# Kernel tuning notes

Measured on AMD Instinct MI355X. Metric: run time of the kernel, lower is better.

## Reference

```python
import jax, jax.numpy as jnp
import numpy as np

NX, NY, NZ = 128, 128, 8
N_VOX = NX * NY * NZ
V, C, HF, WF = 6, 64, 116, 200
PAD_H, PAD_W = 928.0, 1600.0  # img_pad_shape (input image after padding)
IMG_H, IMG_W = 928.0, 1600.0  # img_shape used for the valid-flag bounds check


def _make_proj_mats():
    # Structured lidar2img matrices: pinhole intrinsics + 6 yaw-distributed cameras.
    K = np.array([[500.0, 0, 400, 0], [0, 500.0, 232, 0], [0, 0, 1, 0], [0, 0, 0, 1]], dtype=np.float64)
    A = np.array([[0.0, -1, 0], [0, 0, -1], [1, 0, 0]], dtype=np.float64)  # lidar(x fwd,y left,z up)->cam(z fwd)
    mats = []
    for j in range(V):
        yaw = 2.0 * np.pi * j / V
        c, s = np.cos(yaw), np.sin(yaw)
        Rz = np.array([[c, s, 0], [-s, c, 0], [0, 0, 1]])
        T = np.eye(4)
        T[:3, :3] = A @ Rz
        T[:3, 3] = np.array([0.0, -1.0, 0.0])
        mats.append(K @ T)
    return jnp.asarray(np.stack(mats), dtype=jnp.float32)


def setup_inputs() -> dict:
    key = jax.random.key(0)
    k1, k2 = jax.random.split(key)
    x_fov = jax.random.normal(k1, (1, V, C, HF, WF), dtype=jnp.float32)
    lo = jnp.array([-50.0, -50.0, -5.0], jnp.float32)
    span = jnp.array([100.0, 100.0, 8.0], jnp.float32)
    points = jax.random.uniform(k2, (N_VOX, 3), dtype=jnp.float32) * span + lo
    proj_mats = _make_proj_mats()
    return {"x_fov": x_fov, "points": points, "proj_mats": proj_mats}


def _bilinear_sample(feat, px, py):
    # feat [C,HF,WF]; px/py [N] in feature-map pixel coords.
    # Matches F.grid_sample(mode='bilinear', padding_mode='zeros', align_corners=False).
    x0 = jnp.floor(px)
    y0 = jnp.floor(py)
    wx1 = px - x0
    wy1 = py - y0

    def gather(xi, yi, w):
        inb = (xi >= 0) & (xi < WF) & (yi >= 0) & (yi < HF)
        xc = jnp.clip(xi, 0, WF - 1).astype(jnp.int32)
        yc = jnp.clip(yi, 0, HF - 1).astype(jnp.int32)
        return feat[:, yc, xc] * (w * inb)[None, :]  # [C,N]

    return (gather(x0, y0, (1 - wx1) * (1 - wy1))
            + gather(x0 + 1, y0, wx1 * (1 - wy1))
            + gather(x0, y0 + 1, (1 - wx1) * wy1)
            + gather(x0 + 1, y0 + 1, wx1 * wy1))


def _forward(x_fov, points, proj_mats):
    n = points.shape[0]
    # points_cam2img: homogeneous projection, perspective divide
    pts_h = jnp.concatenate([points, jnp.ones((n, 1), points.dtype)], axis=-1)  # [N,4]
    cam = jnp.einsum('vij,nj->vni', proj_mats, pts_h)  # [V,N,4]
    depth = cam[..., 2]
    d_safe = jnp.where(jnp.abs(depth) > 1e-6, depth, 1e-6)
    u = cam[..., 0] / d_safe  # image-plane x in input-image pixels (scale=1, crop=0, no flip)
    v = cam[..., 1] / d_safe
    # valid_flag: in front of camera and inside img_shape
    valid = (depth > 0) & (u > 0) & (u < IMG_W) & (v > 0) & (v < IMG_H)  # [V,N]
    # normalize by img_pad_shape then map to feature-map pixels (align_corners=False)
    px = u / PAD_W * WF - 0.5
    py = v / PAD_H * HF - 0.5
    feats = jax.vmap(_bilinear_sample)(x_fov[0], px, py)  # [V,C,N]
    feats = feats * valid[:, None, :].astype(feats.dtype)
    vol = feats.sum(0)  # [C,N] masked sum over views
    cnt = valid.sum(0).astype(feats.dtype)  # [N]
    vol = jnp.where(cnt > 0, vol, 0.0) / jnp.clip(cnt, 0.001)[None, :]
    # reshape(n_voxels[::-1] + [-1]).permute(3,2,1,0) -> [C,NX,NY,NZ]
    out = jnp.transpose(vol.reshape(C, NZ, NY, NX), (0, 3, 2, 1))
    return out[None]  # [1,C,NX,NY,NZ]


def reference(x_fov, points, proj_mats):
    return _forward(x_fov, points, proj_mats)
```

## Files before the change

### kernel.cpp

```cpp
#include <hip/hip_runtime.h>
#include <hip/hip_bf16.h>
#include <hip/hip_fp16.h>

#define NXv 128
#define NYv 128
#define NZv 8
#define NVOX (NXv * NYv * NZv)
#define NV 6
#define NC 64
#define HFv 116
#define WFv 200
#define PLANE (HFv * WFv)

#define FT_BYTES ((size_t)NV * PLANE * NC * 2)

typedef float v2f __attribute__((ext_vector_type(2)));

__device__ inline unsigned int f2bf(float f) {
  unsigned int x = __float_as_uint(f);
  unsigned int r = x + 0x7fffu + ((x >> 16) & 1u);
  return (r >> 16) & 0xffffu;
}
__device__ inline float bf_lo(unsigned int q) { return __uint_as_float(q << 16); }
__device__ inline float bf_hi(unsigned int q) { return __uint_as_float(q & 0xffff0000u); }
__device__ inline v2f bfpair(unsigned int u) {
  v2f r;
  r.x = __uint_as_float(u << 16);
  r.y = __uint_as_float(u & 0xffff0000u);
  return r;
}

__device__ inline unsigned short f2h_bits(float f) {
  __half h = __float2half(f);
  return *reinterpret_cast<unsigned short*>(&h);
}
__device__ inline float h_bits2f(unsigned short u) {
  __half_raw r; r.x = u;
  __half h = *reinterpret_cast<__half*>(&r);
  return __half2float(h);
}

__global__ __launch_bounds__(256) void transpose_feat_bf16(
    const float* __restrict__ in, unsigned int* __restrict__ out32) {
  __shared__ float tile[64][65];
  const int v  = blockIdx.y;
  const int p0 = blockIdx.x * 64;
  const float* src = in + (size_t)v * NC * PLANE;
  unsigned int* dst = out32 + (size_t)v * PLANE * (NC / 2);
  const int t = threadIdx.x;

#pragma unroll
  for (int i = 0; i < 4; ++i) {
    const int idx = i * 256 + t;
    const int c  = idx >> 4;
    const int p4 = idx & 15;
    const int pp = p0 + p4 * 4;
    if (pp < PLANE) {
      const float4 f = *(const float4*)(src + (size_t)c * PLANE + pp);
      tile[p4 * 4 + 0][c] = f.x;
      tile[p4 * 4 + 1][c] = f.y;
      tile[p4 * 4 + 2][c] = f.z;
      tile[p4 * 4 + 3][c] = f.w;
    }
  }
  __syncthreads();

#pragma unroll
  for (int i = 0; i < 2; ++i) {
    const int idx = i * 256 + t;
    const int p   = idx >> 3;
    const int c8  = idx & 7;
    const int pp  = p0 + p;
    if (pp < PLANE) {
      uint4 w;
      w.x = f2bf(tile[p][c8 * 8 + 0]) | (f2bf(tile[p][c8 * 8 + 1]) << 16);
      w.y = f2bf(tile[p][c8 * 8 + 2]) | (f2bf(tile[p][c8 * 8 + 3]) << 16);
      w.z = f2bf(tile[p][c8 * 8 + 4]) | (f2bf(tile[p][c8 * 8 + 5]) << 16);
      w.w = f2bf(tile[p][c8 * 8 + 6]) | (f2bf(tile[p][c8 * 8 + 7]) << 16);
      *(uint4*)(dst + (size_t)pp * 32 + c8 * 4) = w;
    }
  }
}

__global__ __launch_bounds__(256, 4) void gather_fused(
    const uint4* __restrict__ feat4,
    const float* __restrict__ points,
    const float* __restrict__ proj,
    float* __restrict__ out) {
  __shared__ uint4 pdl_raw[64][NV];
  __shared__ unsigned short tile_h[64][66];
  __shared__ unsigned int vmask[64];
  __shared__ float projl[96];

  const int bi   = blockIdx.x;
  const int xcd  = bi & 7;
  const int r    = bi >> 3;
  const int tid  = xcd * 2 + (r >> 7);
  const int q    = r & 127;
  const int ix   = (tid & 3) * 32 + (q & 31);
  const int iyg  = (tid >> 2) * 4 + (q >> 5);
  const int iy0g = iyg * 8;

  const int t    = threadIdx.x;
  const int lane = t & 63;
  const int wave = t >> 6;

  if (t < 96) projl[t] = proj[t];
  if (t < 64) vmask[t] = 0u;
  __syncthreads();

  {
    const int slot = t & 63;
    const int vb   = t >> 6;
    const int j    = slot >> 3;
    const int iz   = slot & 7;
    const int n    = iz * (NXv * NYv) + (iy0g + j) * NXv + ix;

    const float x = points[n * 3 + 0];
    const float y = points[n * 3 + 1];
    const float z = points[n * 3 + 2];

#pragma unroll
    for (int vo = 0; vo < 2; ++vo) {
      const int v = vb + vo * 4;
      if (v < NV) {
        const float* M = projl + v * 16;
        const float cx = M[0] * x + M[1] * y + M[2]  * z + M[3];
        const float cy = M[4] * x + M[5] * y + M[6]  * z + M[7];
        const float cz = M[8] * x + M[9] * y + M[10] * z + M[11];

        const float dz = (fabsf(cz) > 1e-6f) ? cz : 1e-6f;
        const float u  = cx / dz;
        const float vv = cy / dz;

        const bool valid = (cz > 0.0f) && (u > 0.0f) && (u < 1600.0f) &&
                           (vv > 0.0f) && (vv < 928.0f);
        if (valid) {
          const float px = u  / 1600.0f * 200.0f - 0.5f;
          const float py = vv / 928.0f  * 116.0f - 0.5f;
          const float fx0 = floorf(px);
          const float fy0 = floorf(py);
          const float wx1 = px - fx0;
          const float wy1 = py - fy0;
          const float wx0 = 1.0f - wx1;
          const float wy0 = 1.0f - wy1;
          const int ix0 = (int)fx0;
          const int iy0 = (int)fy0;

          const bool bx0 = (ix0 >= 0) && (ix0 < WFv);
          const bool bx1 = (ix0 + 1 >= 0) && (ix0 + 1 < WFv);
          const bool by0 = (iy0 >= 0) && (iy0 < HFv);
          const bool by1 = (iy0 + 1 >= 0) && (iy0 + 1 < HFv);

          const int xc0 = min(max(ix0, 0), WFv - 1);
          const int xc1 = min(max(ix0 + 1, 0), WFv - 1);
          const int yc0 = min(max(iy0, 0), HFv - 1);
          const int yc1 = min(max(iy0 + 1, 0), HFv - 1);
          const unsigned int p00 = (unsigned int)(yc0 * WFv + xc0);
          const unsigned int p10 = (unsigned int)(yc0 * WFv + xc1);
          const unsigned int p01 = (unsigned int)(yc1 * WFv + xc0);
          const unsigned int p11 = (unsigned int)(yc1 * WFv + xc1);

          uint4 rec;
          rec.x = p00 | (p10 << 16);
          rec.y = p01 | (p11 << 16);
          rec.z = (unsigned int)f2h_bits((bx0 && by0) ? wx0 * wy0 : 0.0f) |
                  ((unsigned int)f2h_bits((bx1 && by0) ? wx1 * wy0 : 0.0f) << 16);
          rec.w = (unsigned int)f2h_bits((bx0 && by1) ? wx0 * wy1 : 0.0f) |
                  ((unsigned int)f2h_bits((bx1 && by1) ? wx1 * wy1 : 0.0f) << 16);
          pdl_raw[slot][v] = rec;
          atomicOr(&vmask[slot], 1u << v);
        } else {
          const uint4 zrec = {0u, 0u, 0u, 0u};
          pdl_raw[slot][v] = zrec;
        }
      }
    }
  }
  __syncthreads();

  const int pg = lane >> 3;
  const int ch = lane & 7;

#pragma unroll
  for (int it = 0; it < 2; ++it) {
    const int sl = pg * 8 + wave * 2 + it;
    const unsigned int m0 = vmask[sl];
    const int mycnt = __popc(m0);
    const int vdead = min(__builtin_ctz(~m0), NV - 1);

    int km = mycnt;
    km = max(km, __shfl_xor(km, 8));
    km = max(km, __shfl_xor(km, 16));
    km = max(km, __shfl_xor(km, 32));

    v2f acc2[4];
#pragma unroll
    for (int j2 = 0; j2 < 4; ++j2) acc2[j2] = (v2f){0.0f, 0.0f};

    unsigned int m = m0;
    for (int k = 0; k < km; ++k) {
      const bool live = (k < mycnt);
      const int v = live ? __builtin_ctz(m | 0x40u) : vdead;
      m &= m - 1;

      const uint4 cur = pdl_raw[sl][v];
      const unsigned int p00 = cur.x & 0xffffu;
      const unsigned int p10 = cur.x >> 16;
      const unsigned int p01 = cur.y & 0xffffu;
      const unsigned int p11 = cur.y >> 16;
      const float w0 = h_bits2f((unsigned short)(cur.z & 0xffffu));
      const float w1 = h_bits2f((unsigned short)(cur.z >> 16));
      const float w2 = h_bits2f((unsigned short)(cur.w & 0xffffu));
      const float w3 = h_bits2f((unsigned short)(cur.w >> 16));

      const uint4* fb = feat4 + (size_t)v * (PLANE * 8) + ch;
      const uint4 q0 = fb[(size_t)p00 * 8];
      const uint4 q1 = fb[(size_t)p10 * 8];
      const uint4 q2 = fb[(size_t)p01 * 8];
      const uint4 q3 = fb[(size_t)p11 * 8];

      const v2f wv0 = (v2f){w0, w0};
      const v2f wv1 = (v2f){w1, w1};
      const v2f wv2 = (v2f){w2, w2};
      const v2f wv3 = (v2f){w3, w3};

      acc2[0] = __builtin_elementwise_fma(wv0, bfpair(q0.x), acc2[0]);
      acc2[1] = __builtin_elementwise_fma(wv0, bfpair(q0.y), acc2[1]);
      acc2[2] = __builtin_elementwise_fma(wv0, bfpair(q0.z), acc2[2]);
      acc2[3] = __builtin_elementwise_fma(wv0, bfpair(q0.w), acc2[3]);

      acc2[0] = __builtin_elementwise_fma(wv1, bfpair(q1.x), acc2[0]);
      acc2[1] = __builtin_elementwise_fma(wv1, bfpair(q1.y), acc2[1]);
      acc2[2] = __builtin_elementwise_fma(wv1, bfpair(q1.z), acc2[2]);
      acc2[3] = __builtin_elementwise_fma(wv1, bfpair(q1.w), acc2[3]);

      acc2[0] = __builtin_elementwise_fma(wv2, bfpair(q2.x), acc2[0]);
      acc2[1] = __builtin_elementwise_fma(wv2, bfpair(q2.y), acc2[1]);
      acc2[2] = __builtin_elementwise_fma(wv2, bfpair(q2.z), acc2[2]);
      acc2[3] = __builtin_elementwise_fma(wv2, bfpair(q2.w), acc2[3]);

      acc2[0] = __builtin_elementwise_fma(wv3, bfpair(q3.x), acc2[0]);
      acc2[1] = __builtin_elementwise_fma(wv3, bfpair(q3.y), acc2[1]);
      acc2[2] = __builtin_elementwise_fma(wv3, bfpair(q3.z), acc2[2]);
      acc2[3] = __builtin_elementwise_fma(wv3, bfpair(q3.w), acc2[3]);
    }

    const float inv = (mycnt > 0) ? 1.0f / (float)mycnt : 0.0f;
#pragma unroll
    for (int j2 = 0; j2 < 4; ++j2) {
      const unsigned int pk =
          (unsigned int)f2h_bits(acc2[j2].x * inv) |
          ((unsigned int)f2h_bits(acc2[j2].y * inv) << 16);
      *(unsigned int*)&tile_h[sl][ch * 8 + j2 * 2] = pk;
    }
  }

  __syncthreads();

  const size_t obase = (size_t)ix * (NYv * NZv) + (size_t)iy0g * NZv + lane;
#pragma unroll
  for (int i = 0; i < 16; ++i) {
    const int c = i * 4 + wave;
    const float val = h_bits2f(tile_h[lane][c]);
    __builtin_nontemporal_store(val, &out[(size_t)c * NVOX + obase]);
  }
}

__global__ __launch_bounds__(256) void sample_fallback(
    const float* __restrict__ feat,
    const float* __restrict__ points,
    const float* __restrict__ proj,
    float* __restrict__ out) {
  const int wave = threadIdx.x >> 6;
  const int lane = threadIdx.x & 63;
  const int n = blockIdx.x * 4 + wave;

  const float x = points[n * 3 + 0];
  const float y = points[n * 3 + 1];
  const float z = points[n * 3 + 2];

  float acc = 0.0f;
  int cnt = 0;

#pragma unroll
  for (int v = 0; v < NV; ++v) {
    const float* M = proj + v * 16;
    const float cx = M[0] * x + M[1] * y + M[2]  * z + M[3];
    const float cy = M[4] * x + M[5] * y + M[6]  * z + M[7];
    const float cz = M[8] * x + M[9] * y + M[10] * z + M[11];
    const float dz = (fabsf(cz) > 1e-6f) ? cz : 1e-6f;
    const float u  = cx / dz;
    const float vv = cy / dz;
    const bool valid = (cz > 0.0f) && (u > 0.0f) && (u < 1600.0f) &&
                       (vv > 0.0f) && (vv < 928.0f);
    if (!valid) continue;
    cnt++;
    const float px = u  / 1600.0f * 200.0f - 0.5f;
    const float py = vv / 928.0f  * 116.0f - 0.5f;
    const float fx0 = floorf(px);
    const float fy0 = floorf(py);
    const float wx1 = px - fx0;
    const float wy1 = py - fy0;
    const float wx0 = 1.0f - wx1;
    const float wy0 = 1.0f - wy1;
    const int ix0 = (int)fx0;
    const int iy0 = (int)fy0;
    const float w00 = wx0 * wy0, w10 = wx1 * wy0, w01 = wx0 * wy1, w11 = wx1 * wy1;
    const float* basev = feat + ((size_t)v * NC + lane) * PLANE;
    auto tap = [&](int xi, int yi, float w) {
      if (xi >= 0 && xi < WFv && yi >= 0 && yi < HFv)
        acc += w * basev[yi * WFv + xi];
    };
    tap(ix0,     iy0,     w00);
    tap(ix0 + 1, iy0,     w10);
    tap(ix0,     iy0 + 1, w01);
    tap(ix0 + 1, iy0 + 1, w11);
  }

  const float scale = (cnt > 0) ? (1.0f / (float)cnt) : 0.0f;
  const int iz  = n >> 14;
  const int rem = n & 16383;
  const int iy  = rem >> 7;
  const int ixx = rem & 127;
  out[(((size_t)lane * NXv + ixx) * NYv + iy) * NZv + iz] = acc * scale;
}

extern "C" void kernel_launch(void* const* d_in, const int* in_sizes, int n_in,
                              void* d_out, int out_size, void* d_ws, size_t ws_size,
                              hipStream_t stream) {
  const float* x_fov  = (const float*)d_in[0];
  const float* points = (const float*)d_in[1];
  const float* proj   = (const float*)d_in[2];
  float* out = (float*)d_out;

  if (ws_size >= FT_BYTES) {
    unsigned int* ft = (unsigned int*)d_ws;
    dim3 tgrid((PLANE + 63) / 64, NV);
    transpose_feat_bf16<<<tgrid, 256, 0, stream>>>(x_fov, ft);
    gather_fused<<<NXv * NYv / 8, 256, 0, stream>>>((const uint4*)ft, points, proj, out);
  } else {
    sample_fallback<<<NVOX / 4, 256, 0, stream>>>(x_fov, points, proj, out);
  }
}
```

Measured before the change: 99.12 us.

## Split bilinear corner gathers across lane pairs and store weights as fp32

After: 100.5 us, median of 2. No clear change (+1.3%).

```diff
diff --git a/kernel.cpp b/kernel.cpp
--- a/kernel.cpp
+++ b/kernel.cpp
@@ -21,8 +21,6 @@
   unsigned int r = x + 0x7fffu + ((x >> 16) & 1u);
   return (r >> 16) & 0xffffu;
 }
-__device__ inline float bf_lo(unsigned int q) { return __uint_as_float(q << 16); }
-__device__ inline float bf_hi(unsigned int q) { return __uint_as_float(q & 0xffff0000u); }
 __device__ inline v2f bfpair(unsigned int u) {
   v2f r;
   r.x = __uint_as_float(u << 16);
@@ -87,7 +85,8 @@
     const float* __restrict__ points,
     const float* __restrict__ proj,
     float* __restrict__ out) {
-  __shared__ uint4 pdl_raw[64][NV];
+  __shared__ uint2  pdl_pix[64][NV];
+  __shared__ float4 pdl_w[64][NV];
   __shared__ unsigned short tile_h[64][66];
   __shared__ unsigned int vmask[64];
   __shared__ float projl[96];
@@ -161,36 +160,42 @@
           const unsigned int p01 = (unsigned int)(yc1 * WFv + xc0);
           const unsigned int p11 = (unsigned int)(yc1 * WFv + xc1);
 
-          uint4 rec;
-          rec.x = p00 | (p10 << 16);
-          rec.y = p01 | (p11 << 16);
-          rec.z = (unsigned int)f2h_bits((bx0 && by0) ? wx0 * wy0 : 0.0f) |
-                  ((unsigned int)f2h_bits((bx1 && by0) ? wx1 * wy0 : 0.0f) << 16);
-          rec.w = (unsigned int)f2h_bits((bx0 && by1) ? wx0 * wy1 : 0.0f) |
-                  ((unsigned int)f2h_bits((bx1 && by1) ? wx1 * wy1 : 0.0f) << 16);
-          pdl_raw[slot][v] = rec;
+          uint2 pix;
+          pix.x = p00 | (p10 << 16);
+          pix.y = p01 | (p11 << 16);
+          float4 wv;
+          wv.x = (bx0 && by0) ? wx0 * wy0 : 0.0f;
+          wv.y = (bx1 && by0) ? wx1 * wy0 : 0.0f;
+          wv.z = (bx0 && by1) ? wx0 * wy1 : 0.0f;
+          wv.w = (bx1 && by1) ? wx1 * wy1 : 0.0f;
+          pdl_pix[slot][v] = pix;
+          pdl_w[slot][v]   = wv;
           atomicOr(&vmask[slot], 1u << v);
         } else {
-          const uint4 zrec = {0u, 0u, 0u, 0u};
-          pdl_raw[slot][v] = zrec;
+          pdl_pix[slot][v] = (uint2){0u, 0u};
+          pdl_w[slot][v]   = (float4){0.0f, 0.0f, 0.0f, 0.0f};
         }
       }
     }
   }
   __syncthreads();
 
-  const int pg = lane >> 3;
-  const int ch = lane & 7;
-
-#pragma unroll
-  for (int it = 0; it < 2; ++it) {
-    const int sl = pg * 8 + wave * 2 + it;
+  const int pg2  = lane >> 4;
+  const int ch   = (lane >> 1) & 7;
+  const int half = lane & 1;
+
+#pragma unroll
+  for (int i = 0; i < 4; ++i) {
+    const int gi = wave * 4 + i;
+    const int jg = gi >> 3;
+    const int iz = gi & 7;
+    const int sl = (jg * 4 + pg2) * 8 + iz;
+
     const unsigned int m0 = vmask[sl];
     const int mycnt = __popc(m0);
     const int vdead = min(__builtin_ctz(~m0), NV - 1);
 
     int km = mycnt;
-    km = max(km, __shfl_xor(km, 8));
     km = max(km, __shfl_xor(km, 16));
     km = max(km, __shfl_xor(km, 32));
 
@@ -204,55 +209,45 @@
       const int v = live ? __builtin_ctz(m | 0x40u) : vdead;
       m &= m - 1;
 
-      const uint4 cur = pdl_raw[sl][v];
-      const unsigned int p00 = cur.x & 0xffffu;
-      const unsigned int p10 = cur.x >> 16;
-      const unsigned int p01 = cur.y & 0xffffu;
-      const unsigned int p11 = cur.y >> 16;
-      const float w0 = h_bits2f((unsigned short)(cur.z & 0xffffu));
-      const float w1 = h_bits2f((unsigned short)(cur.z >> 16));
-      const float w2 = h_bits2f((unsigned short)(cur.w & 0xffffu));
-      const float w3 = h_bits2f((unsigned short)(cur.w >> 16));
+      const uint2 pix = pdl_pix[sl][v];
+      const unsigned int ui = half ? pix.y : pix.x;
+      const unsigned int pa = ui & 0xffffu;
+      const unsigned int pb = ui >> 16;
+      const v2f wp = *((const v2f*)&pdl_w[sl][v] + half);
 
       const uint4* fb = feat4 + (size_t)v * (PLANE * 8) + ch;
-      const uint4 q0 = fb[(size_t)p00 * 8];
-      const uint4 q1 = fb[(size_t)p10 * 8];
-      const uint4 q2 = fb[(size_t)p01 * 8];
-      const uint4 q3 = fb[(size_t)p11 * 8];
-
-      const v2f wv0 = (v2f){w0, w0};
-      const v2f wv1 = (v2f){w1, w1};
-      const v2f wv2 = (v2f){w2, w2};
-      const v2f wv3 = (v2f){w3, w3};
-
-      acc2[0] = __builtin_elementwise_fma(wv0, bfpair(q0.x), acc2[0]);
-      acc2[1] = __builtin_elementwise_fma(wv0, bfpair(q0.y), acc2[1]);
-      acc2[2] = __builtin_elementwise_fma(wv0, bfpair(q0.z), acc2[2]);
-      acc2[3] = __builtin_elementwise_fma(wv0, bfpair(q0.w), acc2[3]);
-
-      acc2[0] = __builtin_elementwise_fma(wv1, bfpair(q1.x), acc2[0]);
-      acc2[1] = __builtin_elementwise_fma(wv1, bfpair(q1.y), acc2[1]);
-      acc2[2] = __builtin_elementwise_fma(wv1, bfpair(q1.z), acc2[2]);
-      acc2[3] = __builtin_elementwise_fma(wv1, bfpair(q1.w), acc2[3]);
-
-      acc2[0] = __builtin_elementwise_fma(wv2, bfpair(q2.x), acc2[0]);
-      acc2[1] = __builtin_elementwise_fma(wv2, bfpair(q2.y), acc2[1]);
-      acc2[2] = __builtin_elementwise_fma(wv2, bfpair(q2.z), acc2[2]);
-      acc2[3] = __builtin_elementwise_fma(wv2, bfpair(q2.w), acc2[3]);
-
-      acc2[0] = __builtin_elementwise_fma(wv3, bfpair(q3.x), acc2[0]);
-      acc2[1] = __builtin_elementwise_fma(wv3, bfpair(q3.y), acc2[1]);
-      acc2[2] = __builtin_elementwise_fma(wv3, bfpair(q3.z), acc2[2]);
-      acc2[3] = __builtin_elementwise_fma(wv3, bfpair(q3.w), acc2[3]);
-    }
-
-    const float inv = (mycnt > 0) ? 1.0f / (float)mycnt : 0.0f;
+      const uint4 qa = fb[(size_t)pa * 8];
+      const uint4 qb = fb[(size_t)pb * 8];
+
+      const v2f wva = (v2f){wp.x, wp.x};
+      const v2f wvb = (v2f){wp.y, wp.y};
+
+      acc2[0] = __builtin_elementwise_fma(wva, bfpair(qa.x), acc2[0]);
+      acc2[1] = __builtin_elementwise_fma(wva, bfpair(qa.y), acc2[1]);
+      acc2[2] = __builtin_elementwise_fma(wva, bfpair(qa.z), acc2[2]);
+      acc2[3] = __builtin_elementwise_fma(wva, bfpair(qa.w), acc2[3]);
+
+      acc2[0] = __builtin_elementwise_fma(wvb, bfpair(qb.x), acc2[0]);
+      acc2[1] = __builtin_elementwise_fma(wvb, bfpair(qb.y), acc2[1]);
+      acc2[2] = __builtin_elementwise_fma(wvb, bfpair(qb.z), acc2[2]);
+      acc2[3] = __builtin_elementwise_fma(wvb, bfpair(qb.w), acc2[3]);
+    }
+
 #pragma unroll
     for (int j2 = 0; j2 < 4; ++j2) {
-      const unsigned int pk =
-          (unsigned int)f2h_bits(acc2[j2].x * inv) |
-          ((unsigned int)f2h_bits(acc2[j2].y * inv) << 16);
-      *(unsigned int*)&tile_h[sl][ch * 8 + j2 * 2] = pk;
+      acc2[j2].x += __shfl_xor(acc2[j2].x, 1);
+      acc2[j2].y += __shfl_xor(acc2[j2].y, 1);
+    }
+
+    if (half == 0) {
+      const float inv = (mycnt > 0) ? 1.0f / (float)mycnt : 0.0f;
+#pragma unroll
+      for (int j2 = 0; j2 < 4; ++j2) {
+        const unsigned int pk =
+            (unsigned int)f2h_bits(acc2[j2].x * inv) |
+            ((unsigned int)f2h_bits(acc2[j2].y * inv) << 16);
+        *(unsigned int*)&tile_h[sl][ch * 8 + j2 * 2] = pk;
+      }
     }
   }
 
```
